# Kernel optimization log

Hardware: AMD Instinct MI355X
Metric: run time of the kernel (lower is better)

Reference implementation:

```python
import jax, jax.numpy as jnp
import numpy as np

NOOBJ_LAMBDA = 0.5
COORD_LAMBDA = 5.0


def _cxcywh_to_xyxy(b):
    cx, cy, w, h = b[..., 0], b[..., 1], b[..., 2], b[..., 3]
    return jnp.stack([cx - w / 2, cy - h / 2, cx + w / 2, cy + h / 2], axis=-1)


def _pairwise_iou(a, b):
    # a: [B, N, 4] xyxy (preds), b: [B, M, 4] xyxy (targets) -> [B, N, M]
    lt = jnp.maximum(a[:, :, None, :2], b[:, None, :, :2])
    rb = jnp.minimum(a[:, :, None, 2:], b[:, None, :, 2:])
    wh = jnp.clip(rb - lt, 0.0)
    inter = wh[..., 0] * wh[..., 1]
    area_a = (a[..., 2] - a[..., 0]) * (a[..., 3] - a[..., 1])
    area_b = (b[..., 2] - b[..., 0]) * (b[..., 3] - b[..., 1])
    union = area_a[:, :, None] + area_b[:, None, :] - inter
    return inter / jnp.where(union > 0, union, 1.0)


def setup_inputs() -> dict:
    key = jax.random.key(0)
    kp, kt, km = jax.random.split(key, 3)
    B = 8192
    # positive values so sqrt(w), sqrt(h) is well-defined (as the torch code assumes)
    pred = jax.random.uniform(kp, (B, 7, 7, 30), dtype=jnp.float32, minval=0.05, maxval=1.0)
    target = jax.random.uniform(kt, (B, 7, 7, 30), dtype=jnp.float32, minval=0.05, maxval=1.0)
    # target confidence channel (index 4) is the obj/noobj indicator: 0 or 1
    obj = (jax.random.uniform(km, (B, 7, 7)) < 0.2).astype(jnp.float32)
    target = target.at[..., 4].set(obj)
    return {"pred_tensor": pred, "target_tensor": target}


def reference(pred_tensor, target_tensor):
    B = pred_tensor.shape[0]
    pred = pred_tensor.reshape(B, 49, 30)
    target = target_tensor.reshape(B, 49, 30)

    conf_t = target[..., 4]            # [B,49]
    noobj = conf_t == 0                # [B,49]
    obj = conf_t > 0                   # [B,49]

    # --- no-object confidence loss (channels 4 and 9) ---
    d4 = pred[..., 4] - target[..., 4]
    d9 = pred[..., 9] - target[..., 9]
    noobj_loss = jnp.sum(jnp.where(noobj, d4 * d4 + d9 * d9, 0.0))

    # --- object cells: 2 boxes per cell, padded to all 49 cells with a mask ---
    pb = pred[..., :10].reshape(B, 98, 5)
    tb = target[..., :10].reshape(B, 98, 5)
    box_mask = jnp.repeat(obj, 2, axis=1)  # [B,98]

    p_xyxy = _cxcywh_to_xyxy(pb[..., :4])
    t_xyxy = _cxcywh_to_xyxy(tb[..., :4])
    iou = _pairwise_iou(p_xyxy, t_xyxy)  # [B,98,98]
    pair_mask = box_mask[:, :, None] & box_mask[:, None, :]
    iou = jnp.where(pair_mask, iou, 0.0)
    max_iou = jnp.max(iou, axis=1)       # max over pred boxes, per target box [B,98]
    cmask = (max_iou != 0) & box_mask    # [B,98]

    cm = cmask.astype(pred.dtype)
    # coord (cx,cy) loss
    dxy = pb[..., :2] - tb[..., :2]
    coord_loss_cxcy = jnp.sum(cm * jnp.sum(dxy * dxy, axis=-1))
    # coord (sqrt w, sqrt h) loss
    dwh = jnp.sqrt(pb[..., 2:4]) - jnp.sqrt(tb[..., 2:4])
    coord_loss_wh = jnp.sum(cm * jnp.sum(dwh * dwh, axis=-1))
    # object confidence loss
    dconf = pb[..., 4] - tb[..., 4]
    obj_loss = jnp.sum(cm * dconf * dconf)

    # --- class loss over object cells ---
    dcls = pred[..., 10:] - target[..., 10:]
    cls_loss = jnp.sum(obj.astype(pred.dtype) * jnp.sum(dcls * dcls, axis=-1))

    bsz = jnp.asarray(B, pred.dtype)
    batch_cls_loss = cls_loss / bsz
    batch_obj_loss = (obj_loss + noobj_loss * NOOBJ_LAMBDA) / bsz
    batch_coord_loss = (coord_loss_cxcy + coord_loss_wh) * COORD_LAMBDA / bsz
    batch_loss = batch_cls_loss + batch_obj_loss + batch_coord_loss
    return (batch_loss, batch_cls_loss, batch_obj_loss, batch_coord_loss)
```

## Files before the change

kernel.cpp:

```cpp
#include <hip/hip_runtime.h>

#define CH 30
#define CELLS 49
#define ROWF 1470
#define NPAIR 735
#define NQ4 735
#define WPB 4
#define RPBLK 4
#define HITS 6

__device__ __forceinline__ float waveReduce(float v) {
    #pragma unroll
    for (int o = 32; o > 0; o >>= 1) v += __shfl_xor(v, o, 64);
    return v;
}

__global__ __launch_bounds__(256, 8) void yolo_main(const float* __restrict__ pred,
                                                    const float* __restrict__ targ,
                                                    float* __restrict__ ws, int B,
                                                    int NB) {
    const int w = threadIdx.x >> 6;
    const int lane = threadIdx.x & 63;
    const int h = w & 1;
    const int r0 = blockIdx.x * RPBLK + (w >> 1) * 2;

    __shared__ float4 boxS[WPB][2 * CELLS];
    __shared__ int clist[WPB][CELLS];
    __shared__ float sred[WPB][3];

    float cls = 0.f, objc = 0.f, coord = 0.f;

    if (r0 < B) {
        const int nrows = (B - r0) >= 2 ? 2 : 1;
        const float* P = pred + (size_t)r0 * ROWF;
        const float* T = targ + (size_t)r0 * ROWF;
        unsigned long long m[2] = {0ull, 0ull};

        if (nrows == 2) {
            const float4* P4 = (const float4*)P;
            const float4* T4 = (const float4*)T;

            const int cl = lane < CELLS ? lane : CELLS - 1;
            const float conf0 = T[cl * CH + 4];
            const float conf1 = T[ROWF + cl * CH + 4];

            const int q0 = lane + h * 64;
            const int q0c = q0 < NQ4 ? q0 : NQ4 - 1;
            float4 pa = P4[q0c];
            float4 ta = T4[q0c];

            m[0] = __ballot((lane < CELLS) && (conf0 > 0.f));
            m[1] = __ballot((lane < CELLS) && (conf1 > 0.f));

            #pragma unroll
            for (int it = 0; it < HITS; ++it) {
                float4 pb, tb;
                if (it + 1 < HITS) {
                    const int qn = lane + (2 * (it + 1) + h) * 64;
                    const int qc = qn < NQ4 ? qn : NQ4 - 1;
                    pb = P4[qc];
                    tb = T4[qc];
                }
                const int qq = lane + (2 * it + h) * 64;
                const bool valid = qq < NQ4;
                #pragma unroll
                for (int k = 0; k < 2; ++k) {
                    const int p = 2 * qq + k;
                    const int row = p >= NPAIR ? 1 : 0;
                    const int pr = p - row * NPAIR;
                    const int cell = (pr * 17477) >> 18;
                    const int ch0 = 2 * (pr - cell * 15);
                    const float wobj = (float)((m[row] >> cell) & 1ull);
                    const float px = k ? pa.z : pa.x;
                    const float py = k ? pa.w : pa.y;
                    const float tx = k ? ta.z : ta.x;
                    const float ty = k ? ta.w : ta.y;
                    const float dx = px - tx, dy = py - ty;
                    cls += (valid && ch0 >= 10) ? wobj * (dx * dx + dy * dy) : 0.f;
                    const float nn = (ch0 == 4 ? dx * dx : 0.f)
                                   + (ch0 == 8 ? dy * dy : 0.f);
                    objc += valid ? 0.5f * (1.f - wobj) * nn : 0.f;
                }
                if (it + 1 < HITS) { pa = pb; ta = tb; }
            }

            const unsigned long long mask = m[h];
            const int nBox = 2 * __popcll(mask);
            if (nBox) {
                const float* Pr = P + h * ROWF;
                const float* Tr = T + h * ROWF;
                const bool isObj = (lane < CELLS) && ((mask >> lane) & 1ull);
                if (isObj) clist[w][__popcll(mask & ((1ull << lane) - 1ull))] = lane;

                for (int e = lane; e < nBox; e += 64) {
                    const int c = clist[w][e >> 1];
                    const float* pb = Pr + c * CH + (e & 1) * 5;
                    const float cx = pb[0], cy = pb[1], bw = pb[2], bh = pb[3];
                    boxS[w][e] = make_float4(cx - 0.5f * bw, cy - 0.5f * bh,
                                             cx + 0.5f * bw, cy + 0.5f * bh);
                }

                for (int e = lane; e < nBox; e += 64) {
                    const int c = clist[w][e >> 1];
                    const float* tb = Tr + c * CH + (e & 1) * 5;
                    const float tcx = tb[0], tcy = tb[1], tw = tb[2], th = tb[3];
                    const float tx1 = tcx - 0.5f * tw, ty1 = tcy - 0.5f * th;
                    const float tx2 = tcx + 0.5f * tw, ty2 = tcy + 0.5f * th;
                    const float ta2 = (tx2 - tx1) * (ty2 - ty1);
                    float maxiou = 0.f;
                    for (int i = 0; i < nBox; ++i) {
                        const float4 pb4 = boxS[w][i];
                        const float lx = fmaxf(pb4.x, tx1), ly = fmaxf(pb4.y, ty1);
                        const float rx = fminf(pb4.z, tx2), ry = fminf(pb4.w, ty2);
                        const float iw = fmaxf(rx - lx, 0.f), ih = fmaxf(ry - ly, 0.f);
                        const float inter = iw * ih;
                        const float pa2 = (pb4.z - pb4.x) * (pb4.w - pb4.y);
                        const float un = pa2 + ta2 - inter;
                        const float iou = inter / (un > 0.f ? un : 1.f);
                        maxiou = fmaxf(maxiou, iou);
                    }
                    if (maxiou != 0.f) {
                        const float* pb = Pr + c * CH + (e & 1) * 5;
                        const float dcx = pb[0] - tcx, dcy = pb[1] - tcy;
                        coord += dcx * dcx + dcy * dcy;
                        const float dw = sqrtf(pb[2]) - sqrtf(tw);
                        const float dh = sqrtf(pb[3]) - sqrtf(th);
                        coord += dw * dw + dh * dh;
                        const float dc = pb[4] - tb[4];
                        objc += dc * dc;
                    }
                }
            }
        } else if (h == 0) {
            const float2* P2 = (const float2*)P;
            const float2* T2 = (const float2*)T;
            const int cl = lane < CELLS ? lane : CELLS - 1;
            const float conf = T[cl * CH + 4];
            const bool isObj = (lane < CELLS) && (conf > 0.f);
            const unsigned long long mask = __ballot(isObj);
            for (int j = lane; j < NPAIR; j += 64) {
                const float2 pq = P2[j], tq = T2[j];
                const int cell = (j * 17477) >> 18;
                const int ch0 = 2 * (j - cell * 15);
                const float wobj = (float)((mask >> cell) & 1ull);
                const float dx = pq.x - tq.x, dy = pq.y - tq.y;
                cls += (ch0 >= 10) ? wobj * (dx * dx + dy * dy) : 0.f;
                const float nn = (ch0 == 4 ? dx * dx : 0.f)
                               + (ch0 == 8 ? dy * dy : 0.f);
                objc += 0.5f * (1.f - wobj) * nn;
            }
            const int nBox = 2 * __popcll(mask);
            if (nBox) {
                if (isObj) clist[w][__popcll(mask & ((1ull << lane) - 1ull))] = lane;
                for (int e = lane; e < nBox; e += 64) {
                    const int c = clist[w][e >> 1];
                    const float* pb = P + c * CH + (e & 1) * 5;
                    const float cx = pb[0], cy = pb[1], bw = pb[2], bh = pb[3];
                    boxS[w][e] = make_float4(cx - 0.5f * bw, cy - 0.5f * bh,
                                             cx + 0.5f * bw, cy + 0.5f * bh);
                }
                for (int e = lane; e < nBox; e += 64) {
                    const int c = clist[w][e >> 1];
                    const float* tb = T + c * CH + (e & 1) * 5;
                    const float tcx = tb[0], tcy = tb[1], tw = tb[2], th = tb[3];
                    const float tx1 = tcx - 0.5f * tw, ty1 = tcy - 0.5f * th;
                    const float tx2 = tcx + 0.5f * tw, ty2 = tcy + 0.5f * th;
                    const float ta2 = (tx2 - tx1) * (ty2 - ty1);
                    float maxiou = 0.f;
                    for (int i = 0; i < nBox; ++i) {
                        const float4 pb4 = boxS[w][i];
                        const float lx = fmaxf(pb4.x, tx1), ly = fmaxf(pb4.y, ty1);
                        const float rx = fminf(pb4.z, tx2), ry = fminf(pb4.w, ty2);
                        const float iw = fmaxf(rx - lx, 0.f), ih = fmaxf(ry - ly, 0.f);
                        const float inter = iw * ih;
                        const float pa2 = (pb4.z - pb4.x) * (pb4.w - pb4.y);
                        const float un = pa2 + ta2 - inter;
                        const float iou = inter / (un > 0.f ? un : 1.f);
                        maxiou = fmaxf(maxiou, iou);
                    }
                    if (maxiou != 0.f) {
                        const float* pb = P + c * CH + (e & 1) * 5;
                        const float dcx = pb[0] - tcx, dcy = pb[1] - tcy;
                        coord += dcx * dcx + dcy * dcy;
                        const float dw = sqrtf(pb[2]) - sqrtf(tw);
                        const float dh = sqrtf(pb[3]) - sqrtf(th);
                        coord += dw * dw + dh * dh;
                        const float dc = pb[4] - tb[4];
                        objc += dc * dc;
                    }
                }
            }
        }
    }

    cls = waveReduce(cls); objc = waveReduce(objc); coord = waveReduce(coord);
    if (lane == 0) { sred[w][0] = cls; sred[w][1] = objc; sred[w][2] = coord; }
    __syncthreads();
    if (threadIdx.x == 0) {
        float C = 0.f, O = 0.f, X = 0.f;
        #pragma unroll
        for (int k = 0; k < WPB; ++k) { C += sred[k][0]; O += sred[k][1]; X += sred[k][2]; }
        ws[blockIdx.x] = C;
        ws[NB + blockIdx.x] = O;
        ws[2 * NB + blockIdx.x] = X;
    }
}

__global__ __launch_bounds__(1024) void yolo_reduce(const float* __restrict__ ws,
                                                    float* __restrict__ out,
                                                    int NB, float invB) {
    const int tid = threadIdx.x;
    const int w = tid >> 6, lane = tid & 63;
    float c = 0.f, o = 0.f, x = 0.f;
    for (int i = tid; i < NB; i += 1024) {
        c += ws[i];
        o += ws[NB + i];
        x += ws[2 * NB + i];
    }
    c = waveReduce(c); o = waveReduce(o); x = waveReduce(x);
    __shared__ float sred[16][3];
    if (lane == 0) { sred[w][0] = c; sred[w][1] = o; sred[w][2] = x; }
    __syncthreads();
    if (tid == 0) {
        float C = 0.f, O = 0.f, X = 0.f;
        #pragma unroll
        for (int k = 0; k < 16; ++k) { C += sred[k][0]; O += sred[k][1]; X += sred[k][2]; }
        const float bcls = C * invB;
        const float bobj = O * invB;
        const float bcoord = X * 5.0f * invB;
        out[0] = bcls + bobj + bcoord;
        out[1] = bcls;
        out[2] = bobj;
        out[3] = bcoord;
    }
}

extern "C" void kernel_launch(void* const* d_in, const int* in_sizes, int n_in,
                              void* d_out, int out_size, void* d_ws, size_t ws_size,
                              hipStream_t stream) {
    const float* pred = (const float*)d_in[0];
    const float* targ = (const float*)d_in[1];
    float* ws = (float*)d_ws;
    float* out = (float*)d_out;
    const int B = in_sizes[0] / ROWF;
    const int NB = (B + RPBLK - 1) / RPBLK;

    yolo_main<<<NB, 256, 0, stream>>>(pred, targ, ws, B, NB);
    yolo_reduce<<<1, 1024, 0, stream>>>(ws, out, NB, 1.0f / (float)B);
}
```

Before: 120.6 us.

## Stage object-box fields in LDS during streaming pass, deepen load prefetch

During the coalesced streaming pass, each lane writes the box channels (0-9) of object cells into a shared-memory staging buffer. The IoU and coordinate phase then reads these from LDS instead of issuing scattered global reloads of pred and target. The single-step float4 prefetch becomes a three-deep register ring, and launch bounds drop from 8 to 6 waves per SIMD to make room for the extra registers and shared memory. A block-wide barrier now separates the two phases, which adds a sync point and lowers the occupancy target.

```diff
diff --git a/kernel.cpp b/kernel.cpp
--- a/kernel.cpp
+++ b/kernel.cpp
@@ -8,6 +8,7 @@
 #define WPB 4
 #define RPBLK 4
 #define HITS 6
+#define DEPTH 3
 
 __device__ __forceinline__ float waveReduce(float v) {
     #pragma unroll
@@ -15,26 +16,30 @@
     return v;
 }
 
-__global__ __launch_bounds__(256, 8) void yolo_main(const float* __restrict__ pred,
+__global__ __launch_bounds__(256, 6) void yolo_main(const float* __restrict__ pred,
                                                     const float* __restrict__ targ,
                                                     float* __restrict__ ws, int B,
                                                     int NB) {
     const int w = threadIdx.x >> 6;
     const int lane = threadIdx.x & 63;
     const int h = w & 1;
-    const int r0 = blockIdx.x * RPBLK + (w >> 1) * 2;
-
+    const int g = w >> 1;
+    const int r0 = blockIdx.x * RPBLK + g * 2;
+
+    __shared__ float boxRaw[2][2][2][CELLS][10];
     __shared__ float4 boxS[WPB][2 * CELLS];
     __shared__ int clist[WPB][CELLS];
     __shared__ float sred[WPB][3];
 
     float cls = 0.f, objc = 0.f, coord = 0.f;
+    unsigned long long m[2] = {0ull, 0ull};
+    int nrows = 0;
+
+    const float* P = pred + (size_t)r0 * ROWF;
+    const float* T = targ + (size_t)r0 * ROWF;
 
     if (r0 < B) {
-        const int nrows = (B - r0) >= 2 ? 2 : 1;
-        const float* P = pred + (size_t)r0 * ROWF;
-        const float* T = targ + (size_t)r0 * ROWF;
-        unsigned long long m[2] = {0ull, 0ull};
+        nrows = (B - r0) >= 2 ? 2 : 1;
 
         if (nrows == 2) {
             const float4* P4 = (const float4*)P;
@@ -44,22 +49,28 @@
             const float conf0 = T[cl * CH + 4];
             const float conf1 = T[ROWF + cl * CH + 4];
 
-            const int q0 = lane + h * 64;
-            const int q0c = q0 < NQ4 ? q0 : NQ4 - 1;
-            float4 pa = P4[q0c];
-            float4 ta = T4[q0c];
+            float4 pv[DEPTH], tv[DEPTH];
+            #pragma unroll
+            for (int s = 0; s < DEPTH; ++s) {
+                const int q = lane + (2 * s + h) * 64;
+                const int qc = q < NQ4 ? q : NQ4 - 1;
+                pv[s] = P4[qc];
+                tv[s] = T4[qc];
+            }
 
             m[0] = __ballot((lane < CELLS) && (conf0 > 0.f));
             m[1] = __ballot((lane < CELLS) && (conf1 > 0.f));
 
             #pragma unroll
             for (int it = 0; it < HITS; ++it) {
-                float4 pb, tb;
-                if (it + 1 < HITS) {
-                    const int qn = lane + (2 * (it + 1) + h) * 64;
+                const int slot = it % DEPTH;
+                const float4 pa = pv[slot];
+                const float4 ta = tv[slot];
+                if (it + DEPTH < HITS) {
+                    const int qn = lane + (2 * (it + DEPTH) + h) * 64;
                     const int qc = qn < NQ4 ? qn : NQ4 - 1;
-                    pb = P4[qc];
-                    tb = T4[qc];
+                    pv[slot] = P4[qc];
+                    tv[slot] = T4[qc];
                 }
                 const int qq = lane + (2 * it + h) * 64;
                 const bool valid = qq < NQ4;
@@ -70,7 +81,8 @@
                     const int pr = p - row * NPAIR;
                     const int cell = (pr * 17477) >> 18;
                     const int ch0 = 2 * (pr - cell * 15);
-                    const float wobj = (float)((m[row] >> cell) & 1ull);
+                    const int bit = (int)((m[row] >> cell) & 1ull);
+                    const float wobj = (float)bit;
                     const float px = k ? pa.z : pa.x;
                     const float py = k ? pa.w : pa.y;
                     const float tx = k ? ta.z : ta.x;
@@ -80,54 +92,11 @@
                     const float nn = (ch0 == 4 ? dx * dx : 0.f)
                                    + (ch0 == 8 ? dy * dy : 0.f);
                     objc += valid ? 0.5f * (1.f - wobj) * nn : 0.f;
-                }
-                if (it + 1 < HITS) { pa = pb; ta = tb; }
-            }
-
-            const unsigned long long mask = m[h];
-            const int nBox = 2 * __popcll(mask);
-            if (nBox) {
-                const float* Pr = P + h * ROWF;
-                const float* Tr = T + h * ROWF;
-                const bool isObj = (lane < CELLS) && ((mask >> lane) & 1ull);
-                if (isObj) clist[w][__popcll(mask & ((1ull << lane) - 1ull))] = lane;
-
-                for (int e = lane; e < nBox; e += 64) {
-                    const int c = clist[w][e >> 1];
-                    const float* pb = Pr + c * CH + (e & 1) * 5;
-                    const float cx = pb[0], cy = pb[1], bw = pb[2], bh = pb[3];
-                    boxS[w][e] = make_float4(cx - 0.5f * bw, cy - 0.5f * bh,
-                                             cx + 0.5f * bw, cy + 0.5f * bh);
-                }
-
-                for (int e = lane; e < nBox; e += 64) {
-                    const int c = clist[w][e >> 1];
-                    const float* tb = Tr + c * CH + (e & 1) * 5;
-                    const float tcx = tb[0], tcy = tb[1], tw = tb[2], th = tb[3];
-                    const float tx1 = tcx - 0.5f * tw, ty1 = tcy - 0.5f * th;
-                    const float tx2 = tcx + 0.5f * tw, ty2 = tcy + 0.5f * th;
-                    const float ta2 = (tx2 - tx1) * (ty2 - ty1);
-                    float maxiou = 0.f;
-                    for (int i = 0; i < nBox; ++i) {
-                        const float4 pb4 = boxS[w][i];
-                        const float lx = fmaxf(pb4.x, tx1), ly = fmaxf(pb4.y, ty1);
-                        const float rx = fminf(pb4.z, tx2), ry = fminf(pb4.w, ty2);
-                        const float iw = fmaxf(rx - lx, 0.f), ih = fmaxf(ry - ly, 0.f);
-                        const float inter = iw * ih;
-                        const float pa2 = (pb4.z - pb4.x) * (pb4.w - pb4.y);
-                        const float un = pa2 + ta2 - inter;
-                        const float iou = inter / (un > 0.f ? un : 1.f);
-                        maxiou = fmaxf(maxiou, iou);
-                    }
-                    if (maxiou != 0.f) {
-                        const float* pb = Pr + c * CH + (e & 1) * 5;
-                        const float dcx = pb[0] - tcx, dcy = pb[1] - tcy;
-                        coord += dcx * dcx + dcy * dcy;
-                        const float dw = sqrtf(pb[2]) - sqrtf(tw);
-                        const float dh = sqrtf(pb[3]) - sqrtf(th);
-                        coord += dw * dw + dh * dh;
-                        const float dc = pb[4] - tb[4];
-                        objc += dc * dc;
+                    if (valid && bit && ch0 < 10) {
+                        float* dp = &boxRaw[g][0][row][cell][ch0];
+                        dp[0] = px; dp[1] = py;
+                        float* dt = &boxRaw[g][1][row][cell][ch0];
+                        dt[0] = tx; dt[1] = ty;
                     }
                 }
             }
@@ -193,6 +162,56 @@
         }
     }
 
+    __syncthreads();
+
+    if (r0 < B && nrows == 2) {
+        const unsigned long long mask = m[h];
+        const int nBox = 2 * __popcll(mask);
+        if (nBox) {
+            const bool isObj = (lane < CELLS) && ((mask >> lane) & 1ull);
+            if (isObj) clist[w][__popcll(mask & ((1ull << lane) - 1ull))] = lane;
+
+            for (int e = lane; e < nBox; e += 64) {
+                const int c = clist[w][e >> 1];
+                const float* pb = &boxRaw[g][0][h][c][(e & 1) * 5];
+                const float cx = pb[0], cy = pb[1], bw = pb[2], bh = pb[3];
+                boxS[w][e] = make_float4(cx - 0.5f * bw, cy - 0.5f * bh,
+                                         cx + 0.5f * bw, cy + 0.5f * bh);
+            }
+
+            for (int e = lane; e < nBox; e += 64) {
+                const int c = clist[w][e >> 1];
+                const float* tb = &boxRaw[g][1][h][c][(e & 1) * 5];
+                const float tcx = tb[0], tcy = tb[1], tw = tb[2], th = tb[3];
+                const float tx1 = tcx - 0.5f * tw, ty1 = tcy - 0.5f * th;
+                const float tx2 = tcx + 0.5f * tw, ty2 = tcy + 0.5f * th;
+                const float ta2 = (tx2 - tx1) * (ty2 - ty1);
+                float maxiou = 0.f;
+                for (int i = 0; i < nBox; ++i) {
+                    const float4 pb4 = boxS[w][i];
+                    const float lx = fmaxf(pb4.x, tx1), ly = fmaxf(pb4.y, ty1);
+                    const float rx = fminf(pb4.z, tx2), ry = fminf(pb4.w, ty2);
+                    const float iw = fmaxf(rx - lx, 0.f), ih = fmaxf(ry - ly, 0.f);
+                    const float inter = iw * ih;
+                    const float pa2 = (pb4.z - pb4.x) * (pb4.w - pb4.y);
+                    const float un = pa2 + ta2 - inter;
+                    const float iou = inter / (un > 0.f ? un : 1.f);
+                    maxiou = fmaxf(maxiou, iou);
+                }
+                if (maxiou != 0.f) {
+                    const float* pb = &boxRaw[g][0][h][c][(e & 1) * 5];
+                    const float dcx = pb[0] - tcx, dcy = pb[1] - tcy;
+                    coord += dcx * dcx + dcy * dcy;
+                    const float dw = sqrtf(pb[2]) - sqrtf(tw);
+                    const float dh = sqrtf(pb[3]) - sqrtf(th);
+                    coord += dw * dw + dh * dh;
+                    const float dc = pb[4] - tb[4];
+                    objc += dc * dc;
+                }
+            }
+        }
+    }
+
     cls = waveReduce(cls); objc = waveReduce(objc); coord = waveReduce(coord);
     if (lane == 0) { sred[w][0] = cls; sred[w][1] = objc; sred[w][2] = coord; }
     __syncthreads();
```

New measurement: 135.5 us. +12.4%, slower.
